# Performance work log

Hardware: AMD Instinct MI355X
Metric: run time of the kernel (lower is better)

Reference implementation:

```python
import jax, jax.numpy as jnp
import numpy as np

NEG_SLOPE = 0.2

def _segment_softmax(logits, seg, num_segments):
    m = jax.ops.segment_max(logits, seg, num_segments=num_segments)
    m = jnp.where(jnp.isfinite(m), m, 0.0)
    e = jnp.exp(logits - m[seg])
    s = jax.ops.segment_sum(e, seg, num_segments=num_segments)
    return e / (s[seg] + 1e-16)

def _gat_conv(x, src, dst, W, att_src, att_dst, b):
    # PyG GATConv, heads=1, concat=True, add_self_loops=True
    N = x.shape[0]
    h = x @ W                                   # [N, C]
    a_src = h @ att_src                         # [N]
    a_dst = h @ att_dst                         # [N]
    loop = jnp.arange(N, dtype=src.dtype)
    s = jnp.concatenate([src, loop])            # add self-loops
    d = jnp.concatenate([dst, loop])
    logits = jax.nn.leaky_relu(a_src[s] + a_dst[d], NEG_SLOPE)  # [E+N]
    w = _segment_softmax(logits, d, N)
    out = jax.ops.segment_sum(h[s] * w[:, None], d, num_segments=N)
    return out + b

def _sage_conv(x, src, dst, W_l, W_r, b):
    # PyG SAGEConv, aggr='mean', root_weight=True, normalize=False
    N = x.shape[0]
    agg = jax.ops.segment_sum(x[src], dst, num_segments=N)      # [N, C]
    deg = jax.ops.segment_sum(jnp.ones_like(src, dtype=x.dtype), dst, num_segments=N)
    mean = agg / jnp.maximum(deg, 1.0)[:, None]
    return mean @ W_l + x @ W_r + b

def setup_inputs() -> dict:
    key = jax.random.key(0)
    ks = jax.random.split(key, 12)
    N, E, EL, F_IN, D = 100000, 1000000, 200000, 11, 64
    glorot = lambda k, sh: jax.random.uniform(k, sh, jnp.float32, -1.0, 1.0) * np.sqrt(6.0 / (sh[0] + sh[-1]))
    return {
        "x": jax.random.normal(ks[0], (N, F_IN), jnp.float32),
        "edge_index": jax.random.randint(ks[1], (2, E), 0, N, jnp.int64),
        "edge_label_index": jax.random.randint(ks[2], (2, EL), 0, N, jnp.int64),
        "W_gat": glorot(ks[3], (F_IN, D)),
        "att_src": glorot(ks[4], (D,)),
        "att_dst": glorot(ks[5], (D,)),
        "b_gat": jnp.zeros((D,), jnp.float32),
        "W1_l": glorot(ks[6], (D, D)),
        "W1_r": glorot(ks[7], (D, D)),
        "b1": jnp.zeros((D,), jnp.float32),
        "W2_l": glorot(ks[8], (D, D)),
        "W2_r": glorot(ks[9], (D, D)),
        "b2": jnp.zeros((D,), jnp.float32),
        "alpha": jnp.full((4,), 1.0 / 4.0, jnp.float32),  # num_layers + 1
    }

def reference(x, edge_index, edge_label_index, W_gat, att_src, att_dst, b_gat,
              W1_l, W1_r, b1, W2_l, W2_r, b2, alpha):
    src, dst = edge_index[0], edge_index[1]
    weights = jax.nn.softmax(alpha)
    # Faithful to original get_embedding (note: weights[1] is skipped, as in source)
    h = _gat_conv(x, src, dst, W_gat, att_src, att_dst, b_gat)
    out = h * weights[0]
    h = _sage_conv(h, src, dst, W1_l, W1_r, b1)
    out = out + h * weights[2]
    h = _sage_conv(h, src, dst, W2_l, W2_r, b2)
    out = out + h * weights[3]
    # link prediction: gather + elementwise dot
    return (out[edge_label_index[0]] * out[edge_label_index[1]]).sum(-1)
```

## Files before the change

### kernel.cpp

```cpp
#include <hip/hip_runtime.h>
#include <math.h>
#include <float.h>

#define NEG_SLOPE 0.2f
#define NCHUNK 128

typedef _Float16 half8 __attribute__((ext_vector_type(8)));
typedef float f32x4  __attribute__((ext_vector_type(4)));

__global__ __launch_bounds__(256) void gat_input_kernel(
    const float* __restrict__ x, const float* __restrict__ Wg,
    const float* __restrict__ att_src, const float* __restrict__ att_dst,
    _Float16* __restrict__ Hf, float* __restrict__ a_src, float* __restrict__ a_dst, int N,
    const float* __restrict__ W1l, const float* __restrict__ W1r,
    const float* __restrict__ W2l, const float* __restrict__ W2r,
    _Float16* __restrict__ W1hi, _Float16* __restrict__ W1lo,
    _Float16* __restrict__ W2hi, _Float16* __restrict__ W2lo,
    const float* __restrict__ alpha, float* __restrict__ wsm,
    _Float16* __restrict__ Psent)
{
    if (blockIdx.x < 8) {
        if (blockIdx.x == 0 && threadIdx.x == 0) {
            float m = alpha[0];
            for (int i = 1; i < 4; i++) m = fmaxf(m, alpha[i]);
            float e[4], s = 0.f;
            for (int i = 0; i < 4; i++) { e[i] = expf(alpha[i] - m); s += e[i]; }
            for (int i = 0; i < 4; i++) wsm[i] = e[i] / s;
        }
        int which = blockIdx.x >> 2;
        const float* Wl = which ? W2l : W1l;
        const float* Wr = which ? W2r : W1r;
        _Float16* Whi = which ? W2hi : W1hi;
        _Float16* Wlo = which ? W2lo : W1lo;
        int idx = (blockIdx.x & 3) * 256 + threadIdx.x;
        int kc = idx >> 9, rem = idx & 511;
        int t = rem >> 6, ln = rem & 63;
        int quad = ln >> 4, col16 = ln & 15;
        int c = t * 16 + col16;
        #pragma unroll
        for (int j = 0; j < 8; j++) {
            int k = kc * 32 + quad * 8 + j;
            float w = (c < 64) ? Wl[k * 64 + c] : Wr[k * 64 + (c - 64)];
            _Float16 hi = (_Float16)w;
            _Float16 lo = (_Float16)(w - (float)hi);
            Whi[(size_t)idx * 8 + j] = hi;
            Wlo[(size_t)idx * 8 + j] = lo;
        }
    } else if (blockIdx.x == 8) {
        if (threadIdx.x < 64) Hf[(size_t)N * 64 + threadIdx.x] = (_Float16)0.f;
        else if (threadIdx.x < 128) Psent[(size_t)N * 64 + (threadIdx.x - 64)] = (_Float16)0.f;
        else if (threadIdx.x == 128) a_src[N] = -1e30f;
    }
    __shared__ float Wl[11 * 64];
    int tid = threadIdx.x;
    for (int i = tid; i < 11 * 64; i += 256) Wl[i] = Wg[i];
    __syncthreads();
    int lane = tid & 63;
    int n = blockIdx.x * 4 + (tid >> 6);
    if (n >= N) return;
    float xv = (lane < 11) ? x[n * 11 + lane] : 0.f;
    float acc = 0.f;
    #pragma unroll
    for (int k = 0; k < 11; k++) acc += __shfl(xv, k, 64) * Wl[k * 64 + lane];
    Hf[(size_t)n * 64 + lane] = (_Float16)acc;
    float ps = acc * att_src[lane];
    float pd = acc * att_dst[lane];
    for (int off = 32; off; off >>= 1) {
        ps += __shfl_down(ps, off, 64);
        pd += __shfl_down(pd, off, 64);
    }
    if (lane == 0) { a_src[n] = ps; a_dst[n] = pd; }
}


__global__ __launch_bounds__(1024) void edge_hist_kernel(
    const int* __restrict__ dst, int* __restrict__ hist, int E, int NBK)
{
    __shared__ int c[1024];
    int t = threadIdx.x;
    c[t] = 0;
    __syncthreads();
    int chunk = (E + NCHUNK - 1) / NCHUNK;
    int lo = blockIdx.x * chunk;
    int hi = lo + chunk; if (hi > E) hi = E;
    for (int i = lo + t; i < hi; i += 1024)
        atomicAdd(&c[dst[i] >> 7], 1);
    __syncthreads();
    if (t < NBK) hist[t * NCHUNK + blockIdx.x] = c[t];
}

__global__ __launch_bounds__(1024) void edge_scatter_kernel(
    const int* __restrict__ src, const int* __restrict__ dst,
    const int* __restrict__ rstart, unsigned* __restrict__ ebuf, int E, int NBK)
{
    __shared__ int cur[1024];
    int t = threadIdx.x;
    if (t < NBK) cur[t] = rstart[t * NCHUNK + blockIdx.x];
    __syncthreads();
    int chunk = (E + NCHUNK - 1) / NCHUNK;
    int lo = blockIdx.x * chunk;
    int hi = lo + chunk; if (hi > E) hi = E;
    for (int i = lo + t; i < hi; i += 1024) {
        int d = dst[i];
        int p = atomicAdd(&cur[d >> 7], 1);
        ebuf[p] = ((unsigned)src[i] << 7) | (unsigned)(d & 127);
    }
}

__global__ __launch_bounds__(256) void scan_reduce_kernel(
    const int* __restrict__ v, int* __restrict__ bsum, int M)
{
    __shared__ int s[256];
    int t = threadIdx.x;
    int base = blockIdx.x * 1024 + t * 4;
    int sum = 0;
    #pragma unroll
    for (int j = 0; j < 4; j++) { int idx = base + j; if (idx < M) sum += v[idx]; }
    s[t] = sum; __syncthreads();
    for (int off = 128; off; off >>= 1) {
        if (t < off) s[t] += s[t + off];
        __syncthreads();
    }
    if (t == 0) bsum[blockIdx.x] = s[0];
}

__global__ __launch_bounds__(256) void scan_apply_kernel(
    const int* __restrict__ v, const int* __restrict__ bsum,
    int* __restrict__ out, int M, int NB)
{
    __shared__ int s[256];
    int t = threadIdx.x;
    int bv = (t < NB) ? bsum[t] : 0;
    s[t] = bv; __syncthreads();
    for (int off = 1; off < 256; off <<= 1) {
        int xx = (t >= off) ? s[t - off] : 0;
        __syncthreads();
        s[t] += xx;
        __syncthreads();
    }
    int blockoff = (blockIdx.x == 0) ? 0 : s[blockIdx.x - 1];
    __syncthreads();
    int base = blockIdx.x * 1024;
    int vv[4]; int sum = 0;
    #pragma unroll
    for (int j = 0; j < 4; j++) {
        int idx = base + t * 4 + j;
        vv[j] = (idx < M) ? v[idx] : 0;
        sum += vv[j];
    }
    s[t] = sum; __syncthreads();
    for (int off = 1; off < 256; off <<= 1) {
        int xx = (t >= off) ? s[t - off] : 0;
        __syncthreads();
        s[t] += xx;
        __syncthreads();
    }
    int ex = s[t] - sum + blockoff;
    #pragma unroll
    for (int j = 0; j < 4; j++) {
        int idx = base + t * 4 + j;
        if (idx < M) out[idx] = ex;
        ex += vv[j];
    }
}

__global__ __launch_bounds__(256) void bucket_build_kernel(
    const unsigned* __restrict__ ebuf, const int* __restrict__ rstart,
    int* __restrict__ cnt, int* __restrict__ rowstart,
    int* __restrict__ csr, int E, int N, int NBK)
{
    __shared__ int c[128];
    __shared__ int rs[128];
    __shared__ int cur[128];
    int b = blockIdx.x, t = threadIdx.x;
    if (t < 128) { c[t] = 0; cur[t] = 0; }
    __syncthreads();
    int beg = rstart[b * NCHUNK];
    int end = (b == NBK - 1) ? E : rstart[(b + 1) * NCHUNK];
    int n = end - beg;
    int pbeg = beg + 384 * b;
    for (int j = t; j < n; j += 256)
        atomicAdd(&c[ebuf[beg + j] & 127u], 1);
    __syncthreads();
    int myc = (t < 128) ? c[t] : 0;
    int mypc = (myc + 3) & ~3;
    if (t < 128) rs[t] = mypc;
    __syncthreads();
    for (int off = 1; off < 128; off <<= 1) {
        int v = (t < 128 && t >= off) ? rs[t - off] : 0;
        __syncthreads();
        if (t < 128) rs[t] += v;
        __syncthreads();
    }
    int ex = (t < 128) ? (rs[t] - mypc) : 0;
    __syncthreads();
    if (t < 128) rs[t] = ex;
    int base = b << 7;
    if (t < 128 && base + t < N) {
        cnt[base + t] = myc;
        rowstart[base + t] = pbeg + ex;
    }
    __syncthreads();
    for (int j = t; j < n; j += 256) {
        unsigned e = ebuf[beg + j];
        int d = (int)(e & 127u);
        int p = atomicAdd(&cur[d], 1);
        csr[pbeg + rs[d] + p] = (int)(e >> 7);
    }
    __syncthreads();
    if (t < 128) {
        for (int k = myc; k < mypc; k++) csr[pbeg + rs[t] + k] = N;
    }
}

__global__ __launch_bounds__(256) void gat_gather_kernel(
    const _Float16* __restrict__ Hf, const float* __restrict__ a_src,
    const float* __restrict__ a_dst, const float* __restrict__ bg,
    const int* __restrict__ rowstart, const int* __restrict__ cnt,
    const int* __restrict__ csr, const float* __restrict__ wsm,
    _Float16* __restrict__ HG, _Float16* __restrict__ outD, int N)
{
    const half8* __restrict__ H8 = (const half8*)Hf;
    int tid = threadIdx.x;
    int lane = tid & 63;
    int g = lane >> 3, sub = lane & 7;
    int gl = g << 3;
    int d = blockIdx.x * 32 + (tid >> 3);
    if (d >= N) return;
    float ad = a_dst[d];
    int beg = rowstart[d], deg = cnt[d];
    int degp = (deg + 3) & ~3;
    float a0 = a_src[d] + ad;
    float lg0 = a0 > 0.f ? a0 : NEG_SLOPE * a0;
    float w_self = expf(lg0);
    half8 hself = H8[(size_t)d * 8 + sub];
    float acc[8];
    #pragma unroll
    for (int c = 0; c < 8; c++) acc[c] = w_self * (float)hself[c];
    float l_lane = 0.f;
    for (int base = 0; base < degp; base += 8) {
        int nvc = degp - base; if (nvc > 8) nvc = 8;
        int sid = (sub < nvc) ? csr[beg + base + sub] : N;
        float aa = a_src[sid] + ad;
        float lgt = aa > 0.f ? aa : NEG_SLOPE * aa;
        float w = expf(lgt);
        l_lane += w;
        int ib[8]; float wb[8];
        #pragma unroll
        for (int j = 0; j < 8; j++) {
            ib[j] = __shfl(sid, gl + j, 64);
            wb[j] = __shfl(w, gl + j, 64);
        }
        half8 v[8];
        #pragma unroll
        for (int j = 0; j < 8; j++) v[j] = H8[(size_t)ib[j] * 8 + sub];
        #pragma unroll
        for (int j = 0; j < 8; j++) {
            #pragma unroll
            for (int c = 0; c < 8; c++) acc[c] += wb[j] * (float)v[j][c];
        }
    }
    #pragma unroll
    for (int off = 1; off < 8; off <<= 1) l_lane += __shfl_xor(l_lane, off, 64);
    float l = l_lane + w_self;
    float inv = 1.0f / (l + 1e-16f);
    float w0s = wsm[0];
    size_t idx = (size_t)d * 8 + sub;
    half8 hg, od;
    #pragma unroll
    for (int c = 0; c < 8; c++) {
        float o = acc[c] * inv + bg[sub * 8 + c];
        hg[c] = (_Float16)o;
        od[c] = (_Float16)(w0s * o);
    }
    ((half8*)HG)[idx] = hg;
    ((half8*)outD)[idx] = od;
}

__global__ __launch_bounds__(256) void sage_gemm_kernel(
    const _Float16* __restrict__ hin,
    const _Float16* __restrict__ Whi, const _Float16* __restrict__ Wlo,
    const float* __restrict__ bvec,
    _Float16* __restrict__ P, _Float16* __restrict__ Q, int N)
{
    int wave = threadIdx.x >> 6, lane = threadIdx.x & 63;
    int base = blockIdx.x * 64 + wave * 16;
    if (base >= N) return;
    int quad = lane >> 4, col16 = lane & 15;
    int m = base + col16;
    int mc = m < N ? m : N - 1;
    const half8* __restrict__ W8hi = (const half8*)Whi;
    const half8* __restrict__ W8lo = (const half8*)Wlo;
    f32x4 acc[8];
    #pragma unroll
    for (int t = 0; t < 8; t++) acc[t] = (f32x4){0.f, 0.f, 0.f, 0.f};
    #pragma unroll
    for (int kc = 0; kc < 2; kc++) {
        half8 a = *(const half8*)(hin + (size_t)mc * 64 + kc * 32 + quad * 8);
        #pragma unroll
        for (int t = 0; t < 8; t++) {
            size_t off = (size_t)(kc * 8 + t) * 64 + lane;
            half8 bhi = W8hi[off];
            half8 blo = W8lo[off];
            acc[t] = __builtin_amdgcn_mfma_f32_16x16x32_f16(a, bhi, acc[t], 0, 0, 0);
            acc[t] = __builtin_amdgcn_mfma_f32_16x16x32_f16(a, blo, acc[t], 0, 0, 0);
        }
    }
    #pragma unroll
    for (int t = 0; t < 8; t++) {
        #pragma unroll
        for (int r = 0; r < 4; r++) {
            int node = base + quad * 4 + r;
            if (node < N) {
                float v = acc[t][r];
                if (t < 4) {
                    P[(size_t)node * 64 + t * 16 + col16] = (_Float16)v;
                } else {
                    int c = (t - 4) * 16 + col16;
                    Q[(size_t)node * 64 + c] = (_Float16)(v + bvec[c]);
                }
            }
        }
    }
}

__global__ __launch_bounds__(256) void sage_post_kernel(
    const _Float16* __restrict__ P, const _Float16* __restrict__ Q,
    const int* __restrict__ rowstart, const int* __restrict__ cnt,
    const int* __restrict__ csr, const float* __restrict__ wsm, int widx,
    _Float16* __restrict__ hout, _Float16* __restrict__ outD, int N)
{
    const half8* __restrict__ P8 = (const half8*)P;
    int tid = threadIdx.x;
    int lane = tid & 63;
    int g = lane >> 3, sub = lane & 7;
    int gl = g << 3;
    int d = blockIdx.x * 32 + (tid >> 3);
    if (d >= N) return;
    int beg = rowstart[d], deg = cnt[d];
    int degp = (deg + 3) & ~3;
    float acc[8];
    #pragma unroll
    for (int c = 0; c < 8; c++) acc[c] = 0.f;
    for (int base = 0; base < degp; base += 8) {
        int nvc = degp - base; if (nvc > 8) nvc = 8;
        int sid = (sub < nvc) ? csr[beg + base + sub] : N;
        int ib[8];
        #pragma unroll
        for (int j = 0; j < 8; j++) ib[j] = __shfl(sid, gl + j, 64);
        half8 v[8];
        #pragma unroll
        for (int j = 0; j < 8; j++) v[j] = P8[(size_t)ib[j] * 8 + sub];
        #pragma unroll
        for (int j = 0; j < 8; j++) {
            #pragma unroll
            for (int c = 0; c < 8; c++) acc[c] += (float)v[j][c];
        }
    }
    float invd = 1.0f / fmaxf((float)deg, 1.0f);
    size_t idx = (size_t)d * 8 + sub;
    half8 q = ((const half8*)Q)[idx];
    half8 od = ((half8*)outD)[idx];
    float w = wsm[widx];
    half8 ho;
    #pragma unroll
    for (int c = 0; c < 8; c++) {
        float o = acc[c] * invd + (float)q[c];
        ho[c] = (_Float16)o;
        od[c] = (_Float16)((float)od[c] + w * o);
    }
    if (hout) ((half8*)hout)[idx] = ho;
    ((half8*)outD)[idx] = od;
}

__global__ __launch_bounds__(256) void link_pred_kernel(
    const int* __restrict__ eli, const _Float16* __restrict__ outf,
    float* __restrict__ out, int EL)
{
    const half8* __restrict__ o8 = (const half8*)outf;
    int e = blockIdx.x * 32 + (threadIdx.x >> 3);
    int sub = threadIdx.x & 7;
    if (e >= EL) return;
    int a = eli[e], b = eli[EL + e];
    half8 pa = o8[(size_t)a * 8 + sub];
    half8 pb = o8[(size_t)b * 8 + sub];
    float p = 0.f;
    #pragma unroll
    for (int c = 0; c < 8; c++) p += (float)pa[c] * (float)pb[c];
    for (int off = 4; off; off >>= 1) p += __shfl_xor(p, off, 64);
    if (sub == 0) out[e] = p;
}

extern "C" void kernel_launch(void* const* d_in, const int* in_sizes, int n_in,
                              void* d_out, int out_size, void* d_ws, size_t ws_size,
                              hipStream_t stream)
{
    const float* x      = (const float*)d_in[0];
    const int*   ei     = (const int*)d_in[1];
    const int*   eli    = (const int*)d_in[2];
    const float* Wg     = (const float*)d_in[3];
    const float* att_s  = (const float*)d_in[4];
    const float* att_d  = (const float*)d_in[5];
    const float* bg     = (const float*)d_in[6];
    const float* W1l    = (const float*)d_in[7];
    const float* W1r    = (const float*)d_in[8];
    const float* b1     = (const float*)d_in[9];
    const float* W2l    = (const float*)d_in[10];
    const float* W2r    = (const float*)d_in[11];
    const float* b2     = (const float*)d_in[12];
    const float* alpha  = (const float*)d_in[13];

    const int N  = in_sizes[0] / 11;
    const int E  = in_sizes[1] / 2;
    const int EL = in_sizes[2] / 2;
    const int NBK = (N + 127) >> 7;
    const int M   = NBK * NCHUNK;
    const int CSRSZ = E + 384 * NBK;

    const int* src = ei;
    const int* dst = ei + E;

    _Float16* Hf  = (_Float16*)d_ws;
    _Float16* HG  = Hf + (size_t)(N + 1) * 64;
    _Float16* H1  = HG + (size_t)N * 64;
    _Float16* Pt  = H1 + (size_t)N * 64;
    _Float16* Qt  = Pt + (size_t)(N + 1) * 64;
    _Float16* oD  = Qt + (size_t)N * 64;
    _Float16* wf  = oD + (size_t)N * 64;
    _Float16* W1hi = wf;
    _Float16* W1lo = wf + 8192;
    _Float16* W2hi = wf + 16384;
    _Float16* W2lo = wf + 24576;
    float* wsm     = (float*)(wf + 32768);
    float* a_src   = wsm + 4;
    float* a_dst   = a_src + (N + 1);
    int*   cnt     = (int*)(a_dst + N);
    int*   rowstart= cnt + N;
    int*   hist    = rowstart + N;
    int*   rstart  = hist + M;
    int*   bsum    = rstart + M;
    int*   csr     = bsum + 256;
    unsigned* ebuf = (unsigned*)Pt;

    gat_input_kernel<<<(N + 3) / 4, 256, 0, stream>>>(x, Wg, att_s, att_d, Hf, a_src, a_dst, N,
                                                      W1l, W1r, W2l, W2r,
                                                      W1hi, W1lo, W2hi, W2lo, alpha, wsm, Pt);

    edge_hist_kernel<<<NCHUNK, 1024, 0, stream>>>(dst, hist, E, NBK);
    int NB = (M + 1023) / 1024;
    scan_reduce_kernel<<<NB, 256, 0, stream>>>(hist, bsum, M);
    scan_apply_kernel<<<NB, 256, 0, stream>>>(hist, bsum, rstart, M, NB);
    edge_scatter_kernel<<<NCHUNK, 1024, 0, stream>>>(src, dst, rstart, ebuf, E, NBK);
    bucket_build_kernel<<<NBK, 256, 0, stream>>>(ebuf, rstart, cnt, rowstart, csr, E, N, NBK);

    gat_gather_kernel<<<(N + 31) / 32, 256, 0, stream>>>(Hf, a_src, a_dst, bg,
                                                         rowstart, cnt, csr, wsm, HG, oD, N);

    sage_gemm_kernel<<<(N + 63) / 64, 256, 0, stream>>>(HG, W1hi, W1lo, b1, Pt, Qt, N);
    sage_post_kernel<<<(N + 31) / 32, 256, 0, stream>>>(Pt, Qt, rowstart, cnt, csr, wsm, 2, H1, oD, N);

    sage_gemm_kernel<<<(N + 63) / 64, 256, 0, stream>>>(H1, W1hi == W1hi ? W2hi : W2hi, W2lo, b2, Pt, Qt, N);
    sage_post_kernel<<<(N + 31) / 32, 256, 0, stream>>>(Pt, Qt, rowstart, cnt, csr, wsm, 3, nullptr, oD, N);

    link_pred_kernel<<<(EL + 31) / 32, 256, 0, stream>>>(eli, oD, (float*)d_out, EL);
}
```

Measured before the change: 266.7 us.

## Fuse SAGE gather-mean with GEMM via LDS staging, dropping P/Q intermediates

Replaces the separate SAGE GEMM (P=h@Wl, Q=h@Wr+b) and gather-post kernels with one fused kernel per layer. Each block first gathers and averages neighbor features for 64 nodes, then stages [mean | self] rows into swizzled LDS and runs a single K=128 MFMA GEMM against a repacked weight layout. The bias and alpha-weighted output accumulation are applied in an epilogue. This removes the P/Q global round trips and one launch per layer, but it now gathers 64-wide input rows instead of precomputed projections. It also adds LDS usage and block-level syncs.

After: 248.1 us. -7.0%, faster.

```diff
diff --git a/kernel.cpp b/kernel.cpp
--- a/kernel.cpp
+++ b/kernel.cpp
@@ -17,7 +17,7 @@
     _Float16* __restrict__ W1hi, _Float16* __restrict__ W1lo,
     _Float16* __restrict__ W2hi, _Float16* __restrict__ W2lo,
     const float* __restrict__ alpha, float* __restrict__ wsm,
-    _Float16* __restrict__ Psent)
+    _Float16* __restrict__ HG, _Float16* __restrict__ H1)
 {
     if (blockIdx.x < 8) {
         if (blockIdx.x == 0 && threadIdx.x == 0) {
@@ -33,14 +33,14 @@
         _Float16* Whi = which ? W2hi : W1hi;
         _Float16* Wlo = which ? W2lo : W1lo;
         int idx = (blockIdx.x & 3) * 256 + threadIdx.x;
-        int kc = idx >> 9, rem = idx & 511;
+        int kc = idx >> 8, rem = idx & 255;
         int t = rem >> 6, ln = rem & 63;
         int quad = ln >> 4, col16 = ln & 15;
         int c = t * 16 + col16;
         #pragma unroll
         for (int j = 0; j < 8; j++) {
             int k = kc * 32 + quad * 8 + j;
-            float w = (c < 64) ? Wl[k * 64 + c] : Wr[k * 64 + (c - 64)];
+            float w = (k < 64) ? Wl[k * 64 + c] : Wr[(k - 64) * 64 + c];
             _Float16 hi = (_Float16)w;
             _Float16 lo = (_Float16)(w - (float)hi);
             Whi[(size_t)idx * 8 + j] = hi;
@@ -48,8 +48,9 @@
         }
     } else if (blockIdx.x == 8) {
         if (threadIdx.x < 64) Hf[(size_t)N * 64 + threadIdx.x] = (_Float16)0.f;
-        else if (threadIdx.x < 128) Psent[(size_t)N * 64 + (threadIdx.x - 64)] = (_Float16)0.f;
-        else if (threadIdx.x == 128) a_src[N] = -1e30f;
+        else if (threadIdx.x < 128) HG[(size_t)N * 64 + (threadIdx.x - 64)] = (_Float16)0.f;
+        else if (threadIdx.x < 192) H1[(size_t)N * 64 + (threadIdx.x - 128)] = (_Float16)0.f;
+        else if (threadIdx.x == 192) a_src[N] = -1e30f;
     }
     __shared__ float Wl[11 * 64];
     int tid = threadIdx.x;
@@ -277,100 +278,118 @@
     ((half8*)outD)[idx] = od;
 }
 
-__global__ __launch_bounds__(256) void sage_gemm_kernel(
-    const _Float16* __restrict__ hin,
+__global__ __launch_bounds__(256) void sage_fused_kernel(
+    const _Float16* __restrict__ Hin,
     const _Float16* __restrict__ Whi, const _Float16* __restrict__ Wlo,
     const float* __restrict__ bvec,
-    _Float16* __restrict__ P, _Float16* __restrict__ Q, int N)
-{
-    int wave = threadIdx.x >> 6, lane = threadIdx.x & 63;
-    int base = blockIdx.x * 64 + wave * 16;
-    if (base >= N) return;
-    int quad = lane >> 4, col16 = lane & 15;
-    int m = base + col16;
-    int mc = m < N ? m : N - 1;
-    const half8* __restrict__ W8hi = (const half8*)Whi;
-    const half8* __restrict__ W8lo = (const half8*)Wlo;
-    f32x4 acc[8];
-    #pragma unroll
-    for (int t = 0; t < 8; t++) acc[t] = (f32x4){0.f, 0.f, 0.f, 0.f};
-    #pragma unroll
-    for (int kc = 0; kc < 2; kc++) {
-        half8 a = *(const half8*)(hin + (size_t)mc * 64 + kc * 32 + quad * 8);
-        #pragma unroll
-        for (int t = 0; t < 8; t++) {
-            size_t off = (size_t)(kc * 8 + t) * 64 + lane;
-            half8 bhi = W8hi[off];
-            half8 blo = W8lo[off];
-            acc[t] = __builtin_amdgcn_mfma_f32_16x16x32_f16(a, bhi, acc[t], 0, 0, 0);
-            acc[t] = __builtin_amdgcn_mfma_f32_16x16x32_f16(a, blo, acc[t], 0, 0, 0);
-        }
-    }
-    #pragma unroll
-    for (int t = 0; t < 8; t++) {
-        #pragma unroll
-        for (int r = 0; r < 4; r++) {
-            int node = base + quad * 4 + r;
-            if (node < N) {
-                float v = acc[t][r];
-                if (t < 4) {
-                    P[(size_t)node * 64 + t * 16 + col16] = (_Float16)v;
-                } else {
-                    int c = (t - 4) * 16 + col16;
-                    Q[(size_t)node * 64 + c] = (_Float16)(v + bvec[c]);
-                }
-            }
-        }
-    }
-}
-
-__global__ __launch_bounds__(256) void sage_post_kernel(
-    const _Float16* __restrict__ P, const _Float16* __restrict__ Q,
     const int* __restrict__ rowstart, const int* __restrict__ cnt,
     const int* __restrict__ csr, const float* __restrict__ wsm, int widx,
     _Float16* __restrict__ hout, _Float16* __restrict__ outD, int N)
 {
-    const half8* __restrict__ P8 = (const half8*)P;
+    __shared__ __align__(16) char smem[64 * 68 * 4];
+    float* Ot = (float*)smem;
+    const half8* __restrict__ H8 = (const half8*)Hin;
     int tid = threadIdx.x;
     int lane = tid & 63;
-    int g = lane >> 3, sub = lane & 7;
+    int nodeBase = blockIdx.x * 64;
+    int sub = tid & 7;
+    int g = lane >> 3;
     int gl = g << 3;
-    int d = blockIdx.x * 32 + (tid >> 3);
-    if (d >= N) return;
-    int beg = rowstart[d], deg = cnt[d];
-    int degp = (deg + 3) & ~3;
-    float acc[8];
-    #pragma unroll
-    for (int c = 0; c < 8; c++) acc[c] = 0.f;
-    for (int base = 0; base < degp; base += 8) {
-        int nvc = degp - base; if (nvc > 8) nvc = 8;
-        int sid = (sub < nvc) ? csr[beg + base + sub] : N;
-        int ib[8];
-        #pragma unroll
-        for (int j = 0; j < 8; j++) ib[j] = __shfl(sid, gl + j, 64);
-        half8 v[8];
-        #pragma unroll
-        for (int j = 0; j < 8; j++) v[j] = P8[(size_t)ib[j] * 8 + sub];
-        #pragma unroll
-        for (int j = 0; j < 8; j++) {
-            #pragma unroll
-            for (int c = 0; c < 8; c++) acc[c] += (float)v[j][c];
-        }
-    }
-    float invd = 1.0f / fmaxf((float)deg, 1.0f);
-    size_t idx = (size_t)d * 8 + sub;
-    half8 q = ((const half8*)Q)[idx];
-    half8 od = ((half8*)outD)[idx];
+
+    #pragma unroll
+    for (int pass = 0; pass < 2; pass++) {
+        int dloc = pass * 32 + (tid >> 3);
+        int d = nodeBase + dloc;
+        float acc[8];
+        #pragma unroll
+        for (int c = 0; c < 8; c++) acc[c] = 0.f;
+        half8 hself;
+        #pragma unroll
+        for (int c = 0; c < 8; c++) hself[c] = (_Float16)0.f;
+        float invd = 0.f;
+        if (d < N) {
+            int beg = rowstart[d], deg = cnt[d];
+            int degp = (deg + 3) & ~3;
+            for (int base2 = 0; base2 < degp; base2 += 8) {
+                int nvc = degp - base2; if (nvc > 8) nvc = 8;
+                int sid = (sub < nvc) ? csr[beg + base2 + sub] : N;
+                int ib[8];
+                #pragma unroll
+                for (int j = 0; j < 8; j++) ib[j] = __shfl(sid, gl + j, 64);
+                half8 v[8];
+                #pragma unroll
+                for (int j = 0; j < 8; j++) v[j] = H8[(size_t)ib[j] * 8 + sub];
+                #pragma unroll
+                for (int j = 0; j < 8; j++) {
+                    #pragma unroll
+                    for (int c = 0; c < 8; c++) acc[c] += (float)v[j][c];
+                }
+            }
+            invd = 1.0f / fmaxf((float)deg, 1.0f);
+            hself = H8[(size_t)d * 8 + sub];
+        }
+        half8 ah;
+        #pragma unroll
+        for (int c = 0; c < 8; c++) ah[c] = (_Float16)(acc[c] * invd);
+        int rbase = dloc * 256;
+        int swz = (dloc & 7) << 4;
+        *(half8*)(smem + ((rbase + sub * 16) ^ swz)) = ah;
+        *(half8*)(smem + ((rbase + 128 + sub * 16) ^ swz)) = hself;
+    }
+    __syncthreads();
+
+    int quad = lane >> 4, col16 = lane & 15;
+    int wave = tid >> 6;
+    int row = wave * 16 + col16;
+    int rswz = (row & 7) << 4;
+    f32x4 accq[4];
+    #pragma unroll
+    for (int t = 0; t < 4; t++) accq[t] = (f32x4){0.f, 0.f, 0.f, 0.f};
+    #pragma unroll
+    for (int kc = 0; kc < 4; kc++) {
+        half8 a = *(const half8*)(smem + ((row * 256 + kc * 64 + quad * 16) ^ rswz));
+        #pragma unroll
+        for (int t = 0; t < 4; t++) {
+            size_t off = (size_t)((kc * 4 + t) * 64 + lane) * 8;
+            half8 bhi = *(const half8*)(Whi + off);
+            half8 blo = *(const half8*)(Wlo + off);
+            accq[t] = __builtin_amdgcn_mfma_f32_16x16x32_f16(a, bhi, accq[t], 0, 0, 0);
+            accq[t] = __builtin_amdgcn_mfma_f32_16x16x32_f16(a, blo, accq[t], 0, 0, 0);
+        }
+    }
+    __syncthreads();
+    #pragma unroll
+    for (int t = 0; t < 4; t++) {
+        #pragma unroll
+        for (int r = 0; r < 4; r++) {
+            Ot[(wave * 16 + quad * 4 + r) * 68 + t * 16 + col16] = accq[t][r];
+        }
+    }
+    __syncthreads();
+
     float w = wsm[widx];
-    half8 ho;
-    #pragma unroll
-    for (int c = 0; c < 8; c++) {
-        float o = acc[c] * invd + (float)q[c];
-        ho[c] = (_Float16)o;
-        od[c] = (_Float16)((float)od[c] + w * o);
-    }
-    if (hout) ((half8*)hout)[idx] = ho;
-    ((half8*)outD)[idx] = od;
+    #pragma unroll
+    for (int pass = 0; pass < 2; pass++) {
+        int dloc = pass * 32 + (tid >> 3);
+        int d = nodeBase + dloc;
+        if (d >= N) continue;
+        size_t idx = (size_t)d * 8 + sub;
+        float4 o0 = *(float4*)&Ot[dloc * 68 + sub * 8];
+        float4 o1 = *(float4*)&Ot[dloc * 68 + sub * 8 + 4];
+        float4 b0 = *(const float4*)&bvec[sub * 8];
+        float4 b1 = *(const float4*)&bvec[sub * 8 + 4];
+        float o[8] = {o0.x + b0.x, o0.y + b0.y, o0.z + b0.z, o0.w + b0.w,
+                      o1.x + b1.x, o1.y + b1.y, o1.z + b1.z, o1.w + b1.w};
+        half8 od = ((half8*)outD)[idx];
+        half8 ho;
+        #pragma unroll
+        for (int c = 0; c < 8; c++) {
+            ho[c] = (_Float16)o[c];
+            od[c] = (_Float16)((float)od[c] + w * o[c]);
+        }
+        if (hout) ((half8*)hout)[idx] = ho;
+        ((half8*)outD)[idx] = od;
+    }
 }
 
 __global__ __launch_bounds__(256) void link_pred_kernel(
@@ -422,10 +441,8 @@
 
     _Float16* Hf  = (_Float16*)d_ws;
     _Float16* HG  = Hf + (size_t)(N + 1) * 64;
-    _Float16* H1  = HG + (size_t)N * 64;
-    _Float16* Pt  = H1 + (size_t)N * 64;
-    _Float16* Qt  = Pt + (size_t)(N + 1) * 64;
-    _Float16* oD  = Qt + (size_t)N * 64;
+    _Float16* H1  = HG + (size_t)(N + 1) * 64;
+    _Float16* oD  = H1 + (size_t)(N + 1) * 64;
     _Float16* wf  = oD + (size_t)N * 64;
     _Float16* W1hi = wf;
     _Float16* W1lo = wf + 8192;
@@ -436,15 +453,16 @@
     float* a_dst   = a_src + (N + 1);
     int*   cnt     = (int*)(a_dst + N);
     int*   rowstart= cnt + N;
-    int*   hist    = rowstart + N;
+    int*   hist    = rowstart + M ? rowstart + N : rowstart + N;
     int*   rstart  = hist + M;
     int*   bsum    = rstart + M;
     int*   csr     = bsum + 256;
-    unsigned* ebuf = (unsigned*)Pt;
+    unsigned* ebuf = (unsigned*)H1;
 
     gat_input_kernel<<<(N + 3) / 4, 256, 0, stream>>>(x, Wg, att_s, att_d, Hf, a_src, a_dst, N,
                                                       W1l, W1r, W2l, W2r,
-                                                      W1hi, W1lo, W2hi, W2lo, alpha, wsm, Pt);
+                                                      W1hi, W1lo, W2hi, W2lo, alpha, wsm,
+                                                      HG, H1);
 
     edge_hist_kernel<<<NCHUNK, 1024, 0, stream>>>(dst, hist, E, NBK);
     int NB = (M + 1023) / 1024;
@@ -456,11 +474,11 @@
     gat_gather_kernel<<<(N + 31) / 32, 256, 0, stream>>>(Hf, a_src, a_dst, bg,
                                                          rowstart, cnt, csr, wsm, HG, oD, N);
 
-    sage_gemm_kernel<<<(N + 63) / 64, 256, 0, stream>>>(HG, W1hi, W1lo, b1, Pt, Qt, N);
-    sage_post_kernel<<<(N + 31) / 32, 256, 0, stream>>>(Pt, Qt, rowstart, cnt, csr, wsm, 2, H1, oD, N);
-
-    sage_gemm_kernel<<<(N + 63) / 64, 256, 0, stream>>>(H1, W1hi == W1hi ? W2hi : W2hi, W2lo, b2, Pt, Qt, N);
-    sage_post_kernel<<<(N + 31) / 32, 256, 0, stream>>>(Pt, Qt, rowstart, cnt, csr, wsm, 3, nullptr, oD, N);
+    sage_fused_kernel<<<(N + 63) / 64, 256, 0, stream>>>(HG, W1hi, W1lo, b1,
+                                                         rowstart, cnt, csr, wsm, 2, H1, oD, N);
+
+    sage_fused_kernel<<<(N + 63) / 64, 256, 0, stream>>>(H1, W2hi, W2lo, b2,
+                                                         rowstart, cnt, csr, wsm, 3, nullptr, oD, N);
 
     link_pred_kernel<<<(EL + 31) / 32, 256, 0, stream>>>(eli, oD, (float*)d_out, EL);
 }
```
